# Kernel tuning notes

Measured on AMD Instinct MI355X. Metric: run time of the kernel, lower is better.

## Reference

```python
import jax, jax.numpy as jnp
import numpy as np

N = 100_000      # nodes
E = 1_600_000    # edges (avg degree 16)
F_IN = 128       # dataset.num_features
H = 128          # hidden
C = 25_000       # num_clusters (~ target_ratio 0.25 * N)
G = 64           # graphs in batch
NCLS = 10        # dataset.num_classes


def _gcn_conv(x, w, b, src, dst, n):
    # PyG GCNConv: add self loops, symmetric normalization deg^-1/2 A_hat deg^-1/2
    h = x @ w  # [n, out]
    deg = jnp.zeros((n,), x.dtype).at[dst].add(1.0) + 1.0  # +1 self loop
    dis = jax.lax.rsqrt(deg)
    norm = dis[src] * dis[dst]  # [E]
    out = jnp.zeros_like(h).at[dst].add(h[src] * norm[:, None])
    out = out + h * (dis * dis)[:, None]  # self-loop term norm_ii = deg_i^-1
    return out + b


def _mean_pool(x, seg, num_seg):
    s = jax.ops.segment_sum(x, seg, num_segments=num_seg)
    cnt = jax.ops.segment_sum(jnp.ones((x.shape[0],), x.dtype), seg, num_segments=num_seg)
    return s / jnp.maximum(cnt, 1.0)[:, None]


def _max_pool(x, seg, num_seg):
    m = jax.ops.segment_max(x, seg, num_segments=num_seg)
    cnt = jax.ops.segment_sum(jnp.ones((x.shape[0],), x.dtype), seg, num_segments=num_seg)
    return jnp.where(cnt[:, None] > 0, m, 0.0)


def setup_inputs() -> dict:
    key = jax.random.key(0)
    ks = jax.random.split(key, 12)
    def glorot(k, shape):
        fan_in = shape[0]
        return (jax.random.normal(k, shape, jnp.float32) / np.sqrt(fan_in)).astype(jnp.float32)
    return {
        "x": jax.random.normal(ks[0], (N, F_IN), jnp.float32),
        "edge_index": jax.random.randint(ks[1], (2, E), 0, N, dtype=jnp.int32).astype(jnp.int64),
        "batch": jnp.sort(jax.random.randint(ks[2], (N,), 0, G, dtype=jnp.int32)).astype(jnp.int64),
        "cluster": jax.random.randint(ks[3], (N,), 0, C, dtype=jnp.int32).astype(jnp.int64),
        "num_clusters": C,
        "num_graphs": G,
        "W1": glorot(ks[4], (F_IN, H)), "b1": jnp.zeros((H,), jnp.float32),
        "W2": glorot(ks[5], (H, H)),   "b2": jnp.zeros((H,), jnp.float32),
        "W3": glorot(ks[6], (H, H)),   "b3": jnp.zeros((H,), jnp.float32),
        "lin1_w": glorot(ks[7], (4 * H, H)), "lin1_b": jnp.zeros((H,), jnp.float32),
        "lin2_w": glorot(ks[8], (H, NCLS)),  "lin2_b": jnp.zeros((NCLS,), jnp.float32),
    }


def reference(x, edge_index, batch, cluster, num_clusters, num_graphs,
              W1, b1, W2, b2, W3, b3, lin1_w, lin1_b, lin2_w, lin2_b):
    n = x.shape[0]
    src, dst = edge_index[0], edge_index[1]
    # conv1 + relu (dropout is identity in eval mode)
    h = jax.nn.relu(_gcn_conv(x, W1, b1, src, dst, n))
    pre_mean = _mean_pool(h, batch, num_graphs)
    pre_max = _max_pool(h, batch, num_graphs)
    # LaCorePooling(aggregate='mean'): segment-mean nodes by cluster id,
    # relabel edges to cluster ids, derive pooled batch vector.
    hp = _mean_pool(h, cluster, num_clusters)            # [C, H]
    src_p, dst_p = cluster[src], cluster[dst]            # pooled edge list
    batch_p = jax.ops.segment_max(batch, cluster, num_segments=num_clusters)
    batch_p = jnp.maximum(batch_p, 0)                    # empty clusters -> graph 0
    # post-pool GCN layers
    hp = jax.nn.relu(_gcn_conv(hp, W2, b2, src_p, dst_p, num_clusters))
    hp = jax.nn.relu(_gcn_conv(hp, W3, b3, src_p, dst_p, num_clusters))
    post_mean = _mean_pool(hp, batch_p, num_graphs)
    post_max = _max_pool(hp, batch_p, num_graphs)
    z = jnp.concatenate([pre_mean, pre_max, post_mean, post_max], axis=-1)  # [G, 4H]
    z = jax.nn.relu(z @ lin1_w + lin1_b)
    z = z @ lin2_w + lin2_b
    return jax.nn.log_softmax(z, axis=-1)
```

## Files before the change

### kernel.cpp

```cpp
#include <hip/hip_runtime.h>

constexpr int N_NODES = 100000;
constexpr int N_EDGES = 1600000;
constexpr int N_CLUST = 25000;
constexpr int N_GRAPH = 64;
constexpr int NCLSN   = 10;

constexpr int BKT1_SHIFT = 9;
constexpr int NBKT1 = (N_NODES + 511) / 512;
constexpr int EPB = 4096;
constexpr int NEB = (N_EDGES + EPB - 1) / EPB;
constexpr int SORT_CAP = 12288;

constexpr unsigned PAY_SRC_MASK = 0x1FFFFu;

constexpr int SCAN_BPB = 1024;
constexpr int NB1 = (N_NODES + SCAN_BPB - 1) / SCAN_BPB;
constexpr int NB2 = (N_CLUST + SCAN_BPB - 1) / SCAN_BPB;
constexpr int NB3 = (N_CLUST + SCAN_BPB - 1) / SCAN_BPB;
constexpr int NBT = NB1 + NB2 + NB3;

__device__ __forceinline__ float bf16lo(unsigned u){ return __uint_as_float(u << 16); }
__device__ __forceinline__ float bf16hi(unsigned u){ return __uint_as_float(u & 0xffff0000u); }
__device__ __forceinline__ unsigned bf16_rne(float f){
  unsigned u = __float_as_uint(f);
  return (u + 0x7fffu + ((u >> 16) & 1u)) >> 16;
}
__device__ __forceinline__ unsigned pack2(float lo, float hi){
  return bf16_rne(lo) | (bf16_rne(hi) << 16);
}

typedef short bf16x8 __attribute__((ext_vector_type(8)));
typedef float f32x4  __attribute__((ext_vector_type(4)));

__launch_bounds__(1024)
__global__ void count_kernel(const int* __restrict__ ei, int* __restrict__ bhist){
  __shared__ int h1c[NBKT1];
  int t = threadIdx.x;
  for (int i = t; i < NBKT1; i += 1024) h1c[i] = 0;
  __syncthreads();
  int e0 = blockIdx.x * EPB;
  #pragma unroll
  for (int i = 0; i < EPB / 1024; ++i){
    int e = e0 + i * 1024 + t;
    if (e < N_EDGES) atomicAdd(&h1c[ei[N_EDGES + e] >> BKT1_SHIFT], 1);
  }
  __syncthreads();
  for (int i = t; i < NBKT1; i += 1024) bhist[blockIdx.x * NBKT1 + i] = h1c[i];
}

__launch_bounds__(512)
__global__ void colscan(const int* __restrict__ bhist, int* __restrict__ boffs,
                        int* __restrict__ gcnt1){
  __shared__ int s[512];
  int i = blockIdx.x;
  int t = threadIdx.x;
  int v = (t < NEB) ? bhist[t * NBKT1 + i] : 0;
  s[t] = v; __syncthreads();
  for (int o = 1; o < 512; o <<= 1){
    int a = (t >= o) ? s[t - o] : 0;
    __syncthreads(); s[t] += a; __syncthreads();
  }
  if (t < NEB) boffs[t * NBKT1 + i] = s[t] - v;
  if (t == 511) gcnt1[i] = s[511];
}

__launch_bounds__(256)
__global__ void bucket_scan(const int* __restrict__ gcnt1, int* __restrict__ gbase1){
  __shared__ int s[256];
  int t = threadIdx.x;
  int v = (t < NBKT1) ? gcnt1[t] : 0;
  s[t] = v; __syncthreads();
  for (int off = 1; off < 256; off <<= 1){
    int a = (t >= off) ? s[t - off] : 0;
    __syncthreads(); s[t] += a; __syncthreads();
  }
  if (t < NBKT1) gbase1[t] = s[t] - v;
}

__launch_bounds__(1024)
__global__ void scatter_kernel(const int* __restrict__ ei, const int* __restrict__ gbase1,
                               const int* __restrict__ boffs, unsigned int* __restrict__ stage1){
  __shared__ int gb1[NBKT1];
  __shared__ int cur[NBKT1];
  int t = threadIdx.x, b = blockIdx.x;
  for (int i = t; i < NBKT1; i += 1024){
    gb1[i] = gbase1[i] + boffs[b * NBKT1 + i];
    cur[i] = 0;
  }
  __syncthreads();
  int e0 = b * EPB;
  #pragma unroll
  for (int i = 0; i < EPB / 1024; ++i){
    int e = e0 + i * 1024 + t;
    if (e < N_EDGES){
      int src = ei[e], dst = ei[N_EDGES + e];
      int bk = dst >> BKT1_SHIFT;
      int r = atomicAdd(&cur[bk], 1);
      stage1[gb1[bk] + r] = ((unsigned)(dst & 511) << 17) | (unsigned)src;
    }
  }
}

__launch_bounds__(1024)
__global__ void bucket_sort(const unsigned int* __restrict__ stage, const int* __restrict__ gbase,
                            const int* __restrict__ gcnt, int* __restrict__ outpay,
                            int* __restrict__ deg){
  __shared__ int cnt[512], off[512];
  __shared__ int sorted[SORT_CAP];
  int b = blockIdx.x, t = threadIdx.x;
  int base = gbase[b], n = gcnt[b];
  if (t < 512) cnt[t] = 0;
  __syncthreads();
  for (int i = t; i < n; i += 1024) atomicAdd(&cnt[stage[base + i] >> 17], 1);
  __syncthreads();
  if (t < 512){
    int idx = b * 512 + t;
    if (idx < N_NODES) deg[idx] = cnt[t];
    off[t] = cnt[t];
  }
  __syncthreads();
  for (int s = 1; s < 512; s <<= 1){
    int v = 0;
    if (t < 512 && t >= s) v = off[t - s];
    __syncthreads();
    if (t < 512) off[t] += v;
    __syncthreads();
  }
  if (t < 512) off[t] -= cnt[t];
  __syncthreads();
  if (n <= SORT_CAP){
    for (int i = t; i < n; i += 1024){
      unsigned w = stage[base + i];
      int r = atomicAdd(&off[w >> 17], 1);
      sorted[r] = (int)(w & 0x1FFFFFu);
    }
    __syncthreads();
    for (int i = t; i < n; i += 1024) outpay[base + i] = sorted[i];
  } else {
    for (int i = t; i < n; i += 1024){
      unsigned w = stage[base + i];
      int r = atomicAdd(&off[w >> 17], 1);
      outpay[base + r] = (int)(w & 0x1FFFFFu);
    }
  }
}

__global__ void node_prep(const int* __restrict__ cluster, const int* __restrict__ deg1,
                          int* __restrict__ cntn, int* __restrict__ deg2){
  int v = blockIdx.x * blockDim.x + threadIdx.x;
  if (v < N_NODES){
    int c = cluster[v];
    atomicAdd(&cntn[c], 1);
    atomicAdd(&deg2[c], deg1[v]);
  }
}

__device__ __forceinline__ void seg_select(int b, const int* deg1, const int* cntn,
                                           const int* deg2, const int*& src, int& n, int& base){
  if (b < NB1){ src = deg1; n = N_NODES; base = b * SCAN_BPB; }
  else if (b < NB1 + NB2){ src = cntn; n = N_CLUST; base = (b - NB1) * SCAN_BPB; }
  else { src = deg2; n = N_CLUST; base = (b - NB1 - NB2) * SCAN_BPB; }
}

__launch_bounds__(256)
__global__ void block_sums(const int* __restrict__ deg1, const int* __restrict__ cntn,
                           const int* __restrict__ deg2, int* __restrict__ bsum){
  int b = blockIdx.x;
  const int* src; int n, base;
  seg_select(b, deg1, cntn, deg2, src, n, base);
  int t = threadIdx.x;
  int i0 = base + t * 4;
  int s = 0;
  if (i0 + 3 < n){ int4 v = *(const int4*)&src[i0]; s = v.x + v.y + v.z + v.w; }
  else { for (int j = 0; j < 4; ++j){ int i = i0 + j; if (i < n) s += src[i]; } }
  __shared__ int sh[256];
  sh[t] = s; __syncthreads();
  for (int off = 128; off > 0; off >>= 1){
    if (t < off) sh[t] += sh[t + off];
    __syncthreads();
  }
  if (t == 0) bsum[b] = sh[0];
}

__launch_bounds__(256)
__global__ void scan_bsums(const int* __restrict__ bsum, int* __restrict__ boff,
                           int* __restrict__ rowptr1, int* __restrict__ rowptrn,
                           int* __restrict__ rowptr2){
  __shared__ int s[256];
  int t = threadIdx.x;
  int v = (t < NBT) ? bsum[t] : 0;
  s[t] = v; __syncthreads();
  int seg = (t < NB1) ? 0 : (t < NB1 + NB2 ? 1 : 2);
  for (int off = 1; off < 256; off <<= 1){
    int add = 0;
    if (t >= off){
      int u = t - off;
      int useg = (u < NB1) ? 0 : (u < NB1 + NB2 ? 1 : 2);
      if (useg == seg) add = s[u];
    }
    __syncthreads();
    s[t] += add;
    __syncthreads();
  }
  if (t < NBT) boff[t] = s[t] - v;
  if (t == NB1 - 1)       rowptr1[N_NODES] = s[t];
  if (t == NB1 + NB2 - 1) rowptrn[N_CLUST] = s[t];
  if (t == NBT - 1)       rowptr2[N_CLUST] = s[t];
}

__launch_bounds__(256)
__global__ void scan_final(const int* __restrict__ deg1, const int* __restrict__ cntn,
                           const int* __restrict__ deg2, const int* __restrict__ boff,
                           int* __restrict__ rowptr1, float* __restrict__ dis1,
                           int* __restrict__ rowptrn, int* __restrict__ curn,
                           int* __restrict__ rowptr2, float* __restrict__ dis2){
  int b = blockIdx.x;
  const int* src; int n, base;
  seg_select(b, deg1, cntn, deg2, src, n, base);
  int* rp; int* cur; float* dis;
  if (b < NB1){ rp = rowptr1; cur = nullptr; dis = dis1; }
  else if (b < NB1 + NB2){ rp = rowptrn; cur = curn; dis = nullptr; }
  else { rp = rowptr2; cur = nullptr; dis = dis2; }
  int t = threadIdx.x;
  int i0 = base + t * 4;
  int v[4]; int s = 0;
  #pragma unroll
  for (int j = 0; j < 4; ++j){ int i = i0 + j; v[j] = (i < n) ? src[i] : 0; s += v[j]; }
  __shared__ int sh[256];
  sh[t] = s; __syncthreads();
  for (int off = 1; off < 256; off <<= 1){
    int add = (t >= off) ? sh[t - off] : 0;
    __syncthreads();
    sh[t] += add;
    __syncthreads();
  }
  int run = sh[t] - s + boff[b];
  #pragma unroll
  for (int j = 0; j < 4; ++j){
    int i = i0 + j;
    if (i < n){
      rp[i] = run;
      if (cur) cur[i] = run;
      if (dis) dis[i] = rsqrtf((float)v[j] + 1.0f);
      run += v[j];
    }
  }
}

__global__ void fill_n(const int* __restrict__ cluster, int* __restrict__ curn,
                       int* __restrict__ nidx){
  int v = blockIdx.x * blockDim.x + threadIdx.x;
  if (v >= N_NODES) return;
  nidx[atomicAdd(&curn[cluster[v]], 1)] = v;
}

__launch_bounds__(256)
__global__ void psrc_build(const int* __restrict__ rowptrn, const int* __restrict__ nidx,
                           const int* __restrict__ rowptr1, const int* __restrict__ esrc1,
                           const int* __restrict__ cluster, const int* __restrict__ rowptr2,
                           int* __restrict__ psrcC){
  int c = blockIdx.x * 4 + (threadIdx.x >> 6);
  int l = threadIdx.x & 63;
  int mb = rowptrn[c], me = rowptrn[c + 1];
  int cnt = me - mb;
  int base_l = 0, d_l = 0;
  if (l < cnt){
    int v = nidx[mb + l];
    base_l = rowptr1[v];
    d_l = rowptr1[v + 1] - base_l;
  }
  int pref = d_l;
  #pragma unroll
  for (int off = 1; off < 64; off <<= 1){
    int u = __shfl_up(pref, off);
    if (l >= off) pref += u;
  }
  int total = __shfl(pref, 63);
  int wbase = rowptr2[c];
  int dbits = (c & 15) << 17;
  int iters = (total + 63) >> 6;
  for (int k = 0; k < iters; ++k){
    int idx = k * 64 + l;
    int idxc = min(idx, total - 1);
    int m = 0;
    for (int j = 0; j < cnt; ++j){
      int pj = __shfl(pref, j);
      if (idxc >= pj) m = j + 1;
    }
    int pm = __shfl(pref, m);
    int dm = __shfl(d_l, m);
    int bm = __shfl(base_l, m);
    int e = bm + idxc - (pm - dm);
    int sc = cluster[esrc1[e] & (int)PAY_SRC_MASK];
    if (idx < total) psrcC[wbase + idx] = sc | dbits;
  }
}

template<bool A_BF16>
__launch_bounds__(256)
__global__ void gemm_mfma(const void* __restrict__ Aptr, const float* __restrict__ B,
                          const float* __restrict__ scale, unsigned* __restrict__ Cmat,
                          int M){
  __shared__ __align__(16) unsigned Blds[128 * 68];
  __shared__ __align__(16) unsigned Alds[64 * 68];
  const int t = threadIdx.x;
  const int row0 = blockIdx.x * 64;

  #pragma unroll
  for (int i = 0; i < 8; ++i){
    int task = t + i * 256;
    int kp = task >> 5, nq = task & 31;
    float4 b0 = *(const float4*)&B[(2 * kp) * 128 + nq * 4];
    float4 b1 = *(const float4*)&B[(2 * kp + 1) * 128 + nq * 4];
    Blds[(nq * 4 + 0) * 68 + kp] = pack2(b0.x, b1.x);
    Blds[(nq * 4 + 1) * 68 + kp] = pack2(b0.y, b1.y);
    Blds[(nq * 4 + 2) * 68 + kp] = pack2(b0.z, b1.z);
    Blds[(nq * 4 + 3) * 68 + kp] = pack2(b0.w, b1.w);
  }
  if (A_BF16){
    const unsigned* A = (const unsigned*)Aptr;
    #pragma unroll
    for (int i = 0; i < 8; ++i){
      int idx = t + i * 256;
      int row = idx >> 5, c2 = idx & 31;
      int grow = min(row0 + row, M - 1);
      uint2 v = *(const uint2*)&A[(size_t)grow * 64 + c2 * 2];
      Alds[row * 68 + c2 * 2]     = v.x;
      Alds[row * 68 + c2 * 2 + 1] = v.y;
    }
  } else {
    const float* A = (const float*)Aptr;
    #pragma unroll
    for (int i = 0; i < 8; ++i){
      int idx = t + i * 256;
      int row = idx >> 5, k4 = idx & 31;
      int grow = min(row0 + row, M - 1);
      float4 v = *(const float4*)&A[(size_t)grow * 128 + k4 * 4];
      Alds[row * 68 + k4 * 2]     = pack2(v.x, v.y);
      Alds[row * 68 + k4 * 2 + 1] = pack2(v.z, v.w);
    }
  }
  __syncthreads();

  const int wv = t >> 6, l = t & 63, quad = l >> 4, n16 = l & 15;
  f32x4 acc[8];
  #pragma unroll
  for (int nt = 0; nt < 8; ++nt) acc[nt] = (f32x4){0.f, 0.f, 0.f, 0.f};
  const int arow = wv * 16 + n16;
  #pragma unroll
  for (int ks = 0; ks < 4; ++ks){
    bf16x8 af = *(const bf16x8*)&Alds[arow * 68 + ks * 16 + quad * 4];
    #pragma unroll
    for (int nt = 0; nt < 8; ++nt){
      bf16x8 bfr = *(const bf16x8*)&Blds[(nt * 16 + n16) * 68 + ks * 16 + quad * 4];
      acc[nt] = __builtin_amdgcn_mfma_f32_16x16x32_bf16(af, bfr, acc[nt], 0, 0, 0);
    }
  }
  #pragma unroll
  for (int nt = 0; nt < 8; ++nt){
    #pragma unroll
    for (int r = 0; r < 4; ++r){
      int row = row0 + wv * 16 + quad * 4 + r;
      float sc = scale[min(row, M - 1)];
      float v = acc[nt][r] * sc;
      float vhi = __shfl_xor(v, 1);
      if (((l & 1) == 0) && row < M)
        Cmat[(size_t)row * 64 + nt * 8 + (n16 >> 1)] = pack2(v, vhi);
    }
  }
}

constexpr int BSTR = 17;

__launch_bounds__(256, 4)
__global__ void conv_mfma(const unsigned* __restrict__ Ts, const float* __restrict__ dis,
                          const int* __restrict__ rowptr, const int* __restrict__ epay,
                          const float* __restrict__ bias, unsigned* __restrict__ Hout,
                          int M){
  __shared__ unsigned Blds[4][128 * BSTR];
  const int t = threadIdx.x, wv = t >> 6, l = t & 63;
  const int gi = blockIdx.x * 4 + wv;
  const int base = gi * 16;
  if (base >= M) return;
  const int n16 = l & 15, quad = l >> 4, k32 = l & 31;
  const int beg = rowptr[base];
  const int end = rowptr[min(base + 16, M)];
  const int cnt = end - beg;
  const int selfN = min(16, M - base);
  const int total = cnt + selfN;
  const int nch = (total + 31) >> 5;
  unsigned* Bl = &Blds[wv][0];

  f32x4 acc[8];
  #pragma unroll
  for (int nt = 0; nt < 8; ++nt) acc[nt] = (f32x4){0.f, 0.f, 0.f, 0.f};
  float bv[8];
  #pragma unroll
  for (int nt = 0; nt < 8; ++nt) bv[nt] = bias[nt * 16 + n16];

  auto pay_load = [&](int ch) -> int {
    if (cnt == 0) return 0;
    int ke = min(ch * 32 + k32, cnt - 1);
    return epay[beg + ke];
  };
  auto decode = [&](int ch, int p, int& src, int& d){
    int ke = ch * 32 + k32;
    if (ke < cnt){ src = p & (int)PAY_SRC_MASK; d = (p >> 17) & 15; }
    else {
      int sd = ke - cnt;
      d   = (sd < selfN) ? sd : 31;
      src = (sd < selfN) ? (base + sd) : 0;
    }
  };
  auto issue = [&](int src, uint4* u){
    int s[8];
    #pragma unroll
    for (int i = 0; i < 4; ++i){
      int pp = quad + i * 4;
      s[2 * i]     = __shfl(src, 2 * pp);
      s[2 * i + 1] = __shfl(src, 2 * pp + 1);
    }
    #pragma unroll
    for (int i = 0; i < 8; ++i)
      u[i] = *(const uint4*)&Ts[(size_t)s[i] * 64 + n16 * 4];
  };
  auto stage = [&](const uint4* u){
    #pragma unroll
    for (int i = 0; i < 4; ++i){
      int pp = quad + i * 4;
      uint4 u0 = u[2 * i], u1 = u[2 * i + 1];
      unsigned* wp = Bl + (n16 * 8) * BSTR + pp;
      wp[0 * BSTR] = __builtin_amdgcn_perm(u1.x, u0.x, 0x05040100u);
      wp[1 * BSTR] = __builtin_amdgcn_perm(u1.x, u0.x, 0x07060302u);
      wp[2 * BSTR] = __builtin_amdgcn_perm(u1.y, u0.y, 0x05040100u);
      wp[3 * BSTR] = __builtin_amdgcn_perm(u1.y, u0.y, 0x07060302u);
      wp[4 * BSTR] = __builtin_amdgcn_perm(u1.z, u0.z, 0x05040100u);
      wp[5 * BSTR] = __builtin_amdgcn_perm(u1.z, u0.z, 0x07060302u);
      wp[6 * BSTR] = __builtin_amdgcn_perm(u1.w, u0.w, 0x05040100u);
      wp[7 * BSTR] = __builtin_amdgcn_perm(u1.w, u0.w, 0x07060302u);
    }
  };
  auto compute = [&](int d){
    union { unsigned u[4]; bf16x8 v; } af;
    #pragma unroll
    for (int jj = 0; jj < 4; ++jj){
      int d0 = __shfl(d, quad * 8 + 2 * jj);
      int d1 = __shfl(d, quad * 8 + 2 * jj + 1);
      af.u[jj] = (d0 == n16 ? 0x3F80u : 0u) | (d1 == n16 ? 0x3F800000u : 0u);
    }
    #pragma unroll
    for (int nt = 0; nt < 8; ++nt){
      union { unsigned u[4]; bf16x8 v; } bf;
      const unsigned* rp = Bl + (nt * 16 + n16) * BSTR + quad * 4;
      bf.u[0] = rp[0]; bf.u[1] = rp[1]; bf.u[2] = rp[2]; bf.u[3] = rp[3];
      acc[nt] = __builtin_amdgcn_mfma_f32_16x16x32_bf16(af.v, bf.v, acc[nt], 0, 0, 0);
    }
  };

  uint4 u[8];
  int p = pay_load(0);
  int src_c, d_c;
  decode(0, p, src_c, d_c);
  issue(src_c, u);
  int p_nxt = pay_load(1);
  for (int ch = 0; ch < nch; ++ch){
    stage(u);
    int d_keep = d_c;
    if (ch + 1 < nch){
      int s_n, d_n;
      decode(ch + 1, p_nxt, s_n, d_n);
      issue(s_n, u);
      p_nxt = pay_load(ch + 2);
      d_c = d_n;
    }
    compute(d_keep);
  }

  #pragma unroll
  for (int r = 0; r < 4; ++r){
    int row = base + quad * 4 + r;
    float dsc = dis[min(row, M - 1)];
    #pragma unroll
    for (int nt = 0; nt < 8; ++nt){
      float v = fmaxf(fmaf(dsc, acc[nt][r], bv[nt]), 0.f);
      float vhi = __shfl_xor(v, 1);
      if (((l & 1) == 0) && row < M)
        Hout[(size_t)row * 64 + nt * 8 + (n16 >> 1)] = pack2(v, vhi);
    }
  }
}

__launch_bounds__(256)
__global__ void cluster_gather(const unsigned* __restrict__ h1, const int* __restrict__ rowptrn,
                               const int* __restrict__ nidx, const int* __restrict__ batch,
                               unsigned* __restrict__ hp, int* __restrict__ batchp){
  int c = blockIdx.x * 4 + (threadIdx.x >> 6);
  int l = threadIdx.x & 63;
  int q = l & 15, h = l >> 4;
  int mb = rowptrn[c], me = rowptrn[c + 1];
  float acc[8] = {0.f,0.f,0.f,0.f,0.f,0.f,0.f,0.f};
  int vmax = -1;
  for (int base = mb; base < me; base += 64){
    int n = min(64, me - base);
    int vid = nidx[base + min(l, n - 1)];
    if (l < n) vmax = max(vmax, vid);
    int j = 0;
    for (; j + 8 <= n; j += 8){
      int s0 = __shfl(vid, j + h);
      int s1 = __shfl(vid, j + 4 + h);
      uint4 u0 = *(const uint4*)&h1[(size_t)s0 * 64 + q * 4];
      uint4 u1 = *(const uint4*)&h1[(size_t)s1 * 64 + q * 4];
      acc[0] += bf16lo(u0.x); acc[1] += bf16hi(u0.x);
      acc[2] += bf16lo(u0.y); acc[3] += bf16hi(u0.y);
      acc[4] += bf16lo(u0.z); acc[5] += bf16hi(u0.z);
      acc[6] += bf16lo(u0.w); acc[7] += bf16hi(u0.w);
      acc[0] += bf16lo(u1.x); acc[1] += bf16hi(u1.x);
      acc[2] += bf16lo(u1.y); acc[3] += bf16hi(u1.y);
      acc[4] += bf16lo(u1.z); acc[5] += bf16hi(u1.z);
      acc[6] += bf16lo(u1.w); acc[7] += bf16hi(u1.w);
    }
    for (; j < n; j += 4){
      int ei = j + h;
      int s = __shfl(vid, min(ei, n - 1));
      uint4 u = *(const uint4*)&h1[(size_t)s * 64 + q * 4];
      if (ei < n){
        acc[0] += bf16lo(u.x); acc[1] += bf16hi(u.x);
        acc[2] += bf16lo(u.y); acc[3] += bf16hi(u.y);
        acc[4] += bf16lo(u.z); acc[5] += bf16hi(u.z);
        acc[6] += bf16lo(u.w); acc[7] += bf16hi(u.w);
      }
    }
  }
  #pragma unroll
  for (int k = 0; k < 8; ++k){
    acc[k] += __shfl_xor(acc[k], 16);
    acc[k] += __shfl_xor(acc[k], 32);
  }
  #pragma unroll
  for (int off = 32; off > 0; off >>= 1) vmax = max(vmax, __shfl_xor(vmax, off));
  float inv = 1.0f / (float)max(me - mb, 1);
  if (h == 0){
    uint4 o;
    o.x = pack2(acc[0] * inv, acc[1] * inv);
    o.y = pack2(acc[2] * inv, acc[3] * inv);
    o.z = pack2(acc[4] * inv, acc[5] * inv);
    o.w = pack2(acc[6] * inv, acc[7] * inv);
    *(uint4*)&hp[(size_t)c * 64 + q * 4] = o;
  }
  if (l == 0) batchp[c] = (vmax >= 0) ? batch[vmax] : 0;
}

__global__ void cntp_kernel(const int* __restrict__ batchp, int* __restrict__ cntp){
  int c = blockIdx.x * blockDim.x + threadIdx.x;
  if (c < N_CLUST) atomicAdd(&cntp[batchp[c]], 1);
}

__global__ void scan_cntp(const int* __restrict__ cntp, int* __restrict__ gbasep,
                          int* __restrict__ curp){
  int t = threadIdx.x;
  int v = cntp[t];
  int s = v;
  for (int off = 1; off < 64; off <<= 1){
    int u = __shfl_up(s, off);
    if (t >= off) s += u;
  }
  gbasep[t] = s - v; curp[t] = s - v;
  if (t == 63) gbasep[64] = s;
}

__global__ void fill_c(const int* __restrict__ batchp, int* __restrict__ curp,
                       int* __restrict__ cidx){
  int c = blockIdx.x * blockDim.x + threadIdx.x;
  if (c < N_CLUST) cidx[atomicAdd(&curp[batchp[c]], 1)] = c;
}

__global__ void graph_bounds(const int* __restrict__ batch, int* __restrict__ gstart){
  int g = threadIdx.x;
  if (g > N_GRAPH) return;
  int lo = 0, hi = N_NODES;
  while (lo < hi){ int mid = (lo + hi) >> 1; if (batch[mid] < g) lo = mid + 1; else hi = mid; }
  gstart[g] = lo;
}

__device__ __forceinline__ void atomicMaxPosF(float* addr, float v){
  atomicMax((int*)addr, __float_as_int(v));
}

constexpr int PRE_SPLIT = 8;
__launch_bounds__(256)
__global__ void pre_pool_g(const unsigned* __restrict__ h1, const int* __restrict__ gstart,
                           float* __restrict__ psum, float* __restrict__ pmax){
  int g = blockIdx.x / PRE_SPLIT, sp = blockIdx.x % PRE_SPLIT;
  int t = threadIdx.x, w = t >> 6, l = t & 63;
  int s0 = gstart[g], s1 = gstart[g + 1];
  int n = s1 - s0;
  int per = (n + PRE_SPLIT - 1) / PRE_SPLIT;
  int b0 = s0 + sp * per, b1 = min(b0 + per, s1);
  float2 a0{0.f,0.f}, a1{0.f,0.f}, a2{0.f,0.f}, a3{0.f,0.f};
  float2 mx{0.f,0.f};
  int i = b0 + w;
  for (; i + 12 < b1; i += 16){
    unsigned u0 = h1[(size_t)(i     ) * 64 + l];
    unsigned u1 = h1[(size_t)(i +  4) * 64 + l];
    unsigned u2 = h1[(size_t)(i +  8) * 64 + l];
    unsigned u3 = h1[(size_t)(i + 12) * 64 + l];
    float f0x = bf16lo(u0), f0y = bf16hi(u0);
    float f1x = bf16lo(u1), f1y = bf16hi(u1);
    float f2x = bf16lo(u2), f2y = bf16hi(u2);
    float f3x = bf16lo(u3), f3y = bf16hi(u3);
    a0.x += f0x; a0.y += f0y; a1.x += f1x; a1.y += f1y;
    a2.x += f2x; a2.y += f2y; a3.x += f3x; a3.y += f3y;
    mx.x = fmaxf(fmaxf(mx.x, fmaxf(f0x, f1x)), fmaxf(f2x, f3x));
    mx.y = fmaxf(fmaxf(mx.y, fmaxf(f0y, f1y)), fmaxf(f2y, f3y));
  }
  for (; i < b1; i += 4){
    unsigned u = h1[(size_t)i * 64 + l];
    float fx = bf16lo(u), fy = bf16hi(u);
    a0.x += fx; a0.y += fy;
    mx.x = fmaxf(mx.x, fx); mx.y = fmaxf(mx.y, fy);
  }
  __shared__ float2 ssum[4][64], smax[4][64];
  ssum[w][l] = { a0.x + a1.x + a2.x + a3.x, a0.y + a1.y + a2.y + a3.y };
  smax[w][l] = mx;
  __syncthreads();
  if (w == 0){
    float2 S = ssum[0][l], M = smax[0][l];
    #pragma unroll
    for (int k = 1; k < 4; ++k){
      S.x += ssum[k][l].x; S.y += ssum[k][l].y;
      M.x = fmaxf(M.x, smax[k][l].x); M.y = fmaxf(M.y, smax[k][l].y);
    }
    atomicAdd(&psum[g * 128 + 2 * l], S.x);
    atomicAdd(&psum[g * 128 + 2 * l + 1], S.y);
    atomicMaxPosF(&pmax[g * 128 + 2 * l], M.x);
    atomicMaxPosF(&pmax[g * 128 + 2 * l + 1], M.y);
  }
}

constexpr int POST_SPLIT = 4;
__launch_bounds__(256)
__global__ void post_pool_g(const unsigned* __restrict__ hp3, const int* __restrict__ gbasep,
                            const int* __restrict__ cidx,
                            float* __restrict__ psum, float* __restrict__ pmax){
  int g = blockIdx.x / POST_SPLIT, sp = blockIdx.x % POST_SPLIT;
  int t = threadIdx.x, w = t >> 6, l = t & 63;
  int s0 = gbasep[g], s1 = gbasep[g + 1];
  int n = s1 - s0;
  int per = (n + POST_SPLIT * 4 - 1) / (POST_SPLIT * 4);
  int b0 = s0 + (sp * 4 + w) * per, b1 = min(b0 + per, s1);
  float2 a0{0.f,0.f}, a1{0.f,0.f}, a2{0.f,0.f}, a3{0.f,0.f};
  float2 mx{0.f,0.f};
  for (int base = b0; base < b1; base += 64){
    int nn = min(64, b1 - base);
    int cid = cidx[base + min(l, nn - 1)];
    int j = 0;
    for (; j + 4 <= nn; j += 4){
      int c0 = __shfl(cid, j);
      int c1 = __shfl(cid, j + 1);
      int c2 = __shfl(cid, j + 2);
      int c3 = __shfl(cid, j + 3);
      unsigned u0 = hp3[(size_t)c0 * 64 + l];
      unsigned u1 = hp3[(size_t)c1 * 64 + l];
      unsigned u2 = hp3[(size_t)c2 * 64 + l];
      unsigned u3 = hp3[(size_t)c3 * 64 + l];
      float f0x = bf16lo(u0), f0y = bf16hi(u0);
      float f1x = bf16lo(u1), f1y = bf16hi(u1);
      float f2x = bf16lo(u2), f2y = bf16hi(u2);
      float f3x = bf16lo(u3), f3y = bf16hi(u3);
      a0.x += f0x; a0.y += f0y; a1.x += f1x; a1.y += f1y;
      a2.x += f2x; a2.y += f2y; a3.x += f3x; a3.y += f3y;
      mx.x = fmaxf(fmaxf(mx.x, fmaxf(f0x, f1x)), fmaxf(f2x, f3x));
      mx.y = fmaxf(fmaxf(mx.y, fmaxf(f0y, f1y)), fmaxf(f2y, f3y));
    }
    for (; j < nn; ++j){
      int c = __shfl(cid, j);
      unsigned u = hp3[(size_t)c * 64 + l];
      float fx = bf16lo(u), fy = bf16hi(u);
      a0.x += fx; a0.y += fy;
      mx.x = fmaxf(mx.x, fx); mx.y = fmaxf(mx.y, fy);
    }
  }
  __shared__ float2 ssum[4][64], smax[4][64];
  ssum[w][l] = { a0.x + a1.x + a2.x + a3.x, a0.y + a1.y + a2.y + a3.y };
  smax[w][l] = mx;
  __syncthreads();
  if (w == 0){
    float2 S = ssum[0][l], M = smax[0][l];
    #pragma unroll
    for (int k = 1; k < 4; ++k){
      S.x += ssum[k][l].x; S.y += ssum[k][l].y;
      M.x = fmaxf(M.x, smax[k][l].x); M.y = fmaxf(M.y, smax[k][l].y);
    }
    atomicAdd(&psum[g * 128 + 2 * l], S.x);
    atomicAdd(&psum[g * 128 + 2 * l + 1], S.y);
    atomicMaxPosF(&pmax[g * 128 + 2 * l], M.x);
    atomicMaxPosF(&pmax[g * 128 + 2 * l + 1], M.y);
  }
}

__launch_bounds__(128)
__global__ void head_kernel(const float* __restrict__ psum, const float* __restrict__ pmax,
                            const float* __restrict__ postsum, const float* __restrict__ postmax,
                            const int* __restrict__ gstart, const int* __restrict__ cntp,
                            const float* __restrict__ l1w, const float* __restrict__ l1b,
                            const float* __restrict__ l2w, const float* __restrict__ l2b,
                            float* __restrict__ out){
  int g = blockIdx.x, t = threadIdx.x;
  __shared__ float z[512];
  __shared__ float a[128];
  __shared__ float logits[16];
  __shared__ float lse_s;
  float cpre  = (float)max(gstart[g + 1] - gstart[g], 1);
  float cpost = fmaxf((float)cntp[g], 1.0f);
  z[t]       = psum[g * 128 + t] / cpre;
  z[128 + t] = pmax[g * 128 + t];
  z[256 + t] = postsum[g * 128 + t] / cpost;
  z[384 + t] = postmax[g * 128 + t];
  __syncthreads();
  float acc = l1b[t];
  #pragma unroll 8
  for (int k = 0; k < 512; ++k) acc = fmaf(z[k], l1w[k * 128 + t], acc);
  a[t] = fmaxf(acc, 0.f);
  __syncthreads();
  if (t < NCLSN){
    float s2 = l2b[t];
    for (int k = 0; k < 128; ++k) s2 = fmaf(a[k], l2w[k * NCLSN + t], s2);
    logits[t] = s2;
  }
  __syncthreads();
  if (t == 0){
    float m = logits[0];
    for (int c = 1; c < NCLSN; ++c) m = fmaxf(m, logits[c]);
    float s = 0.f;
    for (int c = 0; c < NCLSN; ++c) s += expf(logits[c] - m);
    lse_s = m + logf(s);
  }
  __syncthreads();
  if (t < NCLSN) out[g * NCLSN + t] = logits[t] - lse_s;
}

extern "C" void kernel_launch(void* const* d_in, const int* in_sizes, int n_in,
                              void* d_out, int out_size, void* d_ws, size_t ws_size,
                              hipStream_t stream){
  const float* x       = (const float*)d_in[0];
  const int*   ei      = (const int*)  d_in[1];
  const int*   batch   = (const int*)  d_in[2];
  const int*   cluster = (const int*)  d_in[3];
  const float* W1      = (const float*)d_in[6];
  const float* b1      = (const float*)d_in[7];
  const float* W2      = (const float*)d_in[8];
  const float* b2      = (const float*)d_in[9];
  const float* W3      = (const float*)d_in[10];
  const float* b3      = (const float*)d_in[11];
  const float* l1w     = (const float*)d_in[12];
  const float* l1b     = (const float*)d_in[13];
  const float* l2w     = (const float*)d_in[14];
  const float* l2b     = (const float*)d_in[15];
  float* out = (float*)d_out;

  char* base = (char*)d_ws;
  size_t off = 0;
  auto alloc = [&](size_t bytes) -> char* {
    char* p = base + off;
    off += (bytes + 255) & ~size_t(255);
    return p;
  };
  char*  zbase  = base + off;
  int*   cntn   = (int*)  alloc((size_t)N_CLUST * 4);
  int*   deg2   = (int*)  alloc((size_t)N_CLUST * 4);
  int*   cntp   = (int*)  alloc((size_t)N_GRAPH * 4);
  float* pre_s  = (float*)alloc((size_t)N_GRAPH * 128 * 4);
  float* pre_m  = (float*)alloc((size_t)N_GRAPH * 128 * 4);
  float* post_s = (float*)alloc((size_t)N_GRAPH * 128 * 4);
  float* post_m = (float*)alloc((size_t)N_GRAPH * 128 * 4);
  size_t zsize = off;
  unsigned* Ts1   = (unsigned*)alloc((size_t)N_NODES * 64 * 4);
  unsigned* h1    = (unsigned*)alloc((size_t)N_NODES * 64 * 4);
  int*   esrc1   = (int*)  alloc((size_t)N_EDGES * 4);
  int*   psrcC   = (int*)  alloc((size_t)N_EDGES * 4);
  int*   deg1    = (int*)  alloc((size_t)N_NODES * 4);
  int*   rowptr1 = (int*)  alloc((size_t)(N_NODES + 1) * 4);
  int*   rowptrn = (int*)  alloc((size_t)(N_CLUST + 1) * 4);
  int*   curn    = (int*)  alloc((size_t)N_CLUST * 4);
  int*   rowptr2 = (int*)  alloc((size_t)(N_CLUST + 1) * 4);
  int*   nidx    = (int*)  alloc((size_t)N_NODES * 4);
  float* dis1    = (float*)alloc((size_t)N_NODES * 4);
  float* dis2    = (float*)alloc((size_t)N_CLUST * 4);
  int*   batchp  = (int*)  alloc((size_t)N_CLUST * 4);
  int*   gstart  = (int*)  alloc((size_t)(N_GRAPH + 1) * 4);
  int*   bsum    = (int*)  alloc((size_t)NBT * 4);
  int*   boff    = (int*)  alloc((size_t)NBT * 4);
  int*   gcnt1   = (int*)  alloc((size_t)NBKT1 * 4);
  int*   gbase1  = (int*)  alloc((size_t)NBKT1 * 4);
  int*   bhist   = (int*)  alloc((size_t)NEB * NBKT1 * 4);
  int*   boffs   = (int*)  alloc((size_t)NEB * NBKT1 * 4);
  int*   gbasep  = (int*)  alloc((size_t)(N_GRAPH + 1) * 4);
  int*   curp    = (int*)  alloc((size_t)N_GRAPH * 4);
  int*   cidx    = (int*)  alloc((size_t)N_CLUST * 4);
  unsigned int* stage1 = (unsigned int*)h1;
  unsigned* hp  = Ts1;
  unsigned* Ts2 = Ts1 + (size_t)N_CLUST * 64;
  unsigned* hp2 = Ts1 + (size_t)2 * N_CLUST * 64;
  unsigned* hp3 = Ts1 + (size_t)3 * N_CLUST * 64;
  unsigned* Ts3 = Ts2;

  (void)in_sizes; (void)n_in; (void)out_size; (void)ws_size;

  hipMemsetAsync(zbase, 0, zsize, stream);

  count_kernel  <<<NEB, 1024, 0, stream>>>(ei, bhist);
  colscan       <<<NBKT1, 512, 0, stream>>>(bhist, boffs, gcnt1);
  bucket_scan   <<<1, 256, 0, stream>>>(gcnt1, gbase1);
  scatter_kernel<<<NEB, 1024, 0, stream>>>(ei, gbase1, boffs, stage1);
  bucket_sort   <<<NBKT1, 1024, 0, stream>>>(stage1, gbase1, gcnt1, esrc1, deg1);
  node_prep<<<(N_NODES + 255) / 256, 256, 0, stream>>>(cluster, deg1, cntn, deg2);
  block_sums <<<NBT, 256, 0, stream>>>(deg1, cntn, deg2, bsum);
  scan_bsums <<<1, 256, 0, stream>>>(bsum, boff, rowptr1, rowptrn, rowptr2);
  scan_final <<<NBT, 256, 0, stream>>>(deg1, cntn, deg2, boff,
                                       rowptr1, dis1, rowptrn, curn, rowptr2, dis2);
  fill_n<<<(N_NODES + 255) / 256, 256, 0, stream>>>(cluster, curn, nidx);
  psrc_build<<<N_CLUST / 4, 256, 0, stream>>>(rowptrn, nidx, rowptr1, esrc1,
                                              cluster, rowptr2, psrcC);

  constexpr int NG1 = N_NODES / 16;
  constexpr int NG2 = (N_CLUST + 15) / 16;
  gemm_mfma<false><<<(N_NODES + 63) / 64, 256, 0, stream>>>(x, W1, dis1, Ts1, N_NODES);
  conv_mfma<<<(NG1 + 3) / 4, 256, 0, stream>>>(Ts1, dis1, rowptr1, esrc1, b1, h1, N_NODES);

  graph_bounds<<<1, 128, 0, stream>>>(batch, gstart);
  pre_pool_g<<<N_GRAPH * PRE_SPLIT, 256, 0, stream>>>(h1, gstart, pre_s, pre_m);

  cluster_gather<<<N_CLUST / 4, 256, 0, stream>>>(h1, rowptrn, nidx, batch, hp, batchp);
  cntp_kernel<<<(N_CLUST + 255) / 256, 256, 0, stream>>>(batchp, cntp);
  scan_cntp<<<1, 64, 0, stream>>>(cntp, gbasep, curp);
  fill_c<<<(N_CLUST + 255) / 256, 256, 0, stream>>>(batchp, curp, cidx);

  gemm_mfma<true><<<(N_CLUST + 63) / 64, 256, 0, stream>>>(hp, W2, dis2, Ts2, N_CLUST);
  conv_mfma<<<(NG2 + 3) / 4, 256, 0, stream>>>(Ts2, dis2, rowptr2, psrcC, b2, hp2, N_CLUST);

  gemm_mfma<true><<<(N_CLUST + 63) / 64, 256, 0, stream>>>(hp2, W3, dis2, Ts3, N_CLUST);
  conv_mfma<<<(NG2 + 3) / 4, 256, 0, stream>>>(Ts3, dis2, rowptr2, psrcC, b3, hp3, N_CLUST);

  post_pool_g<<<N_GRAPH * POST_SPLIT, 256, 0, stream>>>(hp3, gbasep, cidx, post_s, post_m);
  head_kernel<<<N_GRAPH, 128, 0, stream>>>(pre_s, pre_m, post_s, post_m, gstart, cntp,
                                           l1w, l1b, l2w, l2b, out);
}
```

Measured before the change: 610.8 us.

## Split each 16-row conv group's edge chunks across four waves with LDS reduction

Before this change each wave in conv_mfma owned one 16-row destination group and walked all of its edge chunks alone. Now one block owns a group, its four waves take chunks round-robin, and the partial MFMA accumulators are combined through LDS. Each wave then applies bias, scale and ReLU to two of the eight column tiles. The aim is a shorter serial gather chain per group and better latency hiding, especially for the denser pooled graphs. In exchange the block count rises fourfold, every block pays a __syncthreads and an LDS reduction, and waves sit idle when a group has fewer than four chunks.

```diff
diff --git a/kernel.cpp b/kernel.cpp
--- a/kernel.cpp
+++ b/kernel.cpp
@@ -380,9 +380,7 @@
                           int M){
   __shared__ unsigned Blds[4][128 * BSTR];
   const int t = threadIdx.x, wv = t >> 6, l = t & 63;
-  const int gi = blockIdx.x * 4 + wv;
-  const int base = gi * 16;
-  if (base >= M) return;
+  const int base = blockIdx.x * 16;
   const int n16 = l & 15, quad = l >> 4, k32 = l & 31;
   const int beg = rowptr[base];
   const int end = rowptr[min(base + 16, M)];
@@ -395,9 +393,6 @@
   f32x4 acc[8];
   #pragma unroll
   for (int nt = 0; nt < 8; ++nt) acc[nt] = (f32x4){0.f, 0.f, 0.f, 0.f};
-  float bv[8];
-  #pragma unroll
-  for (int nt = 0; nt < 8; ++nt) bv[nt] = bias[nt * 16 + n16];
 
   auto pay_load = [&](int ch) -> int {
     if (cnt == 0) return 0;
@@ -458,32 +453,48 @@
     }
   };
 
-  uint4 u[8];
-  int p = pay_load(0);
-  int src_c, d_c;
-  decode(0, p, src_c, d_c);
-  issue(src_c, u);
-  int p_nxt = pay_load(1);
-  for (int ch = 0; ch < nch; ++ch){
-    stage(u);
-    int d_keep = d_c;
-    if (ch + 1 < nch){
-      int s_n, d_n;
-      decode(ch + 1, p_nxt, s_n, d_n);
-      issue(s_n, u);
-      p_nxt = pay_load(ch + 2);
-      d_c = d_n;
-    }
-    compute(d_keep);
-  }
-
-  #pragma unroll
-  for (int r = 0; r < 4; ++r){
-    int row = base + quad * 4 + r;
-    float dsc = dis[min(row, M - 1)];
-    #pragma unroll
-    for (int nt = 0; nt < 8; ++nt){
-      float v = fmaxf(fmaf(dsc, acc[nt][r], bv[nt]), 0.f);
+  if (wv < nch){
+    uint4 u[8];
+    int p = pay_load(wv);
+    int src_c, d_c;
+    decode(wv, p, src_c, d_c);
+    issue(src_c, u);
+    int p_nxt = pay_load(wv + 4);
+    for (int ch = wv; ch < nch; ch += 4){
+      stage(u);
+      int d_keep = d_c;
+      if (ch + 4 < nch){
+        int s_n, d_n;
+        decode(ch + 4, p_nxt, s_n, d_n);
+        issue(s_n, u);
+        p_nxt = pay_load(ch + 8);
+        d_c = d_n;
+      }
+      compute(d_keep);
+    }
+  }
+
+  constexpr int WSTR = 128 * BSTR;
+  float* F = (float*)&Blds[0][0];
+  float* myF = F + wv * WSTR;
+  #pragma unroll
+  for (int nt = 0; nt < 8; ++nt){
+    #pragma unroll
+    for (int r = 0; r < 4; ++r)
+      myF[(nt * 4 + r) * 64 + l] = acc[nt][r];
+  }
+  __syncthreads();
+  #pragma unroll
+  for (int nt2 = 0; nt2 < 2; ++nt2){
+    int nt = wv * 2 + nt2;
+    float bvv = bias[nt * 16 + n16];
+    #pragma unroll
+    for (int r = 0; r < 4; ++r){
+      int row = base + quad * 4 + r;
+      int idx = (nt * 4 + r) * 64 + l;
+      float s = F[idx] + F[WSTR + idx] + F[2 * WSTR + idx] + F[3 * WSTR + idx];
+      float dsc = dis[min(row, M - 1)];
+      float v = fmaxf(fmaf(dsc, s, bvv), 0.f);
       float vhi = __shfl_xor(v, 1);
       if (((l & 1) == 0) && row < M)
         Hout[(size_t)row * 64 + nt * 8 + (n16 >> 1)] = pack2(v, vhi);
@@ -826,7 +837,7 @@
   constexpr int NG1 = N_NODES / 16;
   constexpr int NG2 = (N_CLUST + 15) / 16;
   gemm_mfma<false><<<(N_NODES + 63) / 64, 256, 0, stream>>>(x, W1, dis1, Ts1, N_NODES);
-  conv_mfma<<<(NG1 + 3) / 4, 256, 0, stream>>>(Ts1, dis1, rowptr1, esrc1, b1, h1, N_NODES);
+  conv_mfma<<<NG1, 256, 0, stream>>>(Ts1, dis1, rowptr1, esrc1, b1, h1, N_NODES);
 
   graph_bounds<<<1, 128, 0, stream>>>(batch, gstart);
   pre_pool_g<<<N_GRAPH * PRE_SPLIT, 256, 0, stream>>>(h1, gstart, pre_s, pre_m);
@@ -837,10 +848,10 @@
   fill_c<<<(N_CLUST + 255) / 256, 256, 0, stream>>>(batchp, curp, cidx);
 
   gemm_mfma<true><<<(N_CLUST + 63) / 64, 256, 0, stream>>>(hp, W2, dis2, Ts2, N_CLUST);
-  conv_mfma<<<(NG2 + 3) / 4, 256, 0, stream>>>(Ts2, dis2, rowptr2, psrcC, b2, hp2, N_CLUST);
+  conv_mfma<<<NG2, 256, 0, stream>>>(Ts2, dis2, rowptr2, psrcC, b2, hp2, N_CLUST);
 
   gemm_mfma<true><<<(N_CLUST + 63) / 64, 256, 0, stream>>>(hp2, W3, dis2, Ts3, N_CLUST);
-  conv_mfma<<<(NG2 + 3) / 4, 256, 0, stream>>>(Ts3, dis2, rowptr2, psrcC, b3, hp3, N_CLUST);
+  conv_mfma<<<NG2, 256, 0, stream>>>(Ts3, dis2, rowptr2, psrcC, b3, hp3, N_CLUST);
 
   post_pool_g<<<N_GRAPH * POST_SPLIT, 256, 0, stream>>>(hp3, gbasep, cidx, post_s, post_m);
   head_kernel<<<N_GRAPH, 128, 0, stream>>>(pre_s, pre_m, post_s, post_m, gstart, cntp,
```

Result: faster. 586.5 us (-4.0%).
